# Optimization experiments

Measured on AMD Instinct MI355X. Metric: run time of the kernel, lower is better.

## Reference

```python
import jax, jax.numpy as jnp
import numpy as np

K_CENTERS = 10
G_CENTERS = 2
EPS = 1e-12  # tf.math.l2_normalize epsilon


def setup_inputs() -> dict:
    key = jax.random.key(0)
    k1, k2, k3 = jax.random.split(key, 3)
    B, H, W, D = 16, 16, 64, 512
    KC = K_CENTERS + G_CENTERS
    feat = jax.random.normal(k1, (B, H, W, D), dtype=jnp.float32)
    cluster_score = jax.random.normal(k2, (B, H, W, KC), dtype=jnp.float32)
    cluster = jax.random.normal(k3, (KC, D), dtype=jnp.float32)
    return {"feat": feat, "cluster_score": cluster_score, "cluster": cluster}


def reference(feat, cluster_score, cluster):
    B, H, W, D = feat.shape
    KC = cluster.shape[0]
    # Softmax over clusters (stable)
    A = jax.nn.softmax(cluster_score, axis=-1)            # [B,H,W,KC]
    # Flatten spatial dims: sum_{s} A[b,s,k] * (feat[b,s,d] - cluster[k,d])
    Af = A.reshape(B, H * W, KC)
    ff = feat.reshape(B, H * W, D)
    # = einsum(A, feat) - (sum_s A)[b,k] * cluster[k,d]  (avoids [B,S,KC,D] intermediate)
    cluster_res = jnp.einsum('bsk,bsd->bkd', Af, ff) - Af.sum(axis=1)[..., None] * cluster[None]
    # GhostVLAD: keep only real clusters
    cluster_res = cluster_res[:, :K_CENTERS, :]           # [B,K,D]
    # L2 normalize over feature dim
    sq = jnp.sum(cluster_res * cluster_res, axis=-1, keepdims=True)
    cluster_l2 = cluster_res * jax.lax.rsqrt(jnp.maximum(sq, EPS))
    return cluster_l2.reshape(B, K_CENTERS * D)
```

## Files before the change

### kernel.cpp

```cpp
#include <hip/hip_runtime.h>
#include <hip/hip_bf16.h>


#define B_   16
#define S_   1024
#define D_   512
#define KC_  12
#define K_   10
#define CH_  16
#define SCH_ (S_ / CH_)
#define NT1  512
#define NPAR 4

__global__ __launch_bounds__(NT1) void vlad_accum(
    const float* __restrict__ feat, const float* __restrict__ score,
    float* __restrict__ part, float* __restrict__ asum_part)
{
    const int bid = blockIdx.x;
    const int b = bid / CH_, c = bid % CH_;
    const int s0 = c * SCH_;
    const int tid = threadIdx.x;
    const int par = tid >> 7;
    const int col = tid & 127;

    __shared__ float A[SCH_][KC_];
    __shared__ float red[NPAR - 1][K_ * 4][128];

    if (tid < SCH_) {
        const float4* sp = (const float4*)(score + (size_t)(b * S_ + s0 + tid) * KC_);
        const float4 w0 = sp[0], w1 = sp[1], w2 = sp[2];
        float x[KC_] = {w0.x, w0.y, w0.z, w0.w, w1.x, w1.y, w1.z, w1.w,
                        w2.x, w2.y, w2.z, w2.w};
        float m = x[0];
        #pragma unroll
        for (int k = 1; k < KC_; k++) m = fmaxf(m, x[k]);
        float sum = 0.f;
        #pragma unroll
        for (int k = 0; k < KC_; k++) { x[k] = __expf(x[k] - m); sum += x[k]; }
        const float inv = 1.0f / sum;
        #pragma unroll
        for (int k = 0; k < KC_; k++) A[tid][k] = x[k] * inv;
    }
    __syncthreads();

    if (tid < K_) {
        float v = 0.f;
        #pragma unroll
        for (int s = 0; s < SCH_; s++) v += A[s][tid];
        asum_part[(b * CH_ + c) * K_ + tid] = v;
    }

    float acc[K_][4];
    #pragma unroll
    for (int k = 0; k < K_; k++)
        acc[k][0] = acc[k][1] = acc[k][2] = acc[k][3] = 0.f;

    const float4* fp = (const float4*)(feat + (size_t)(b * S_ + s0) * D_) + col;
    #pragma unroll 8
    for (int i = 0; i < SCH_ / NPAR; i++) {
        const int s = NPAR * i + par;
        const float4 v = fp[(size_t)s * (D_ / 4)];
        const float4 a0 = *(const float4*)(&A[s][0]);
        const float4 a1 = *(const float4*)(&A[s][4]);
        const float2 a2 = *(const float2*)(&A[s][8]);
        const float a[K_] = {a0.x, a0.y, a0.z, a0.w, a1.x, a1.y, a1.z, a1.w,
                             a2.x, a2.y};
        #pragma unroll
        for (int k = 0; k < K_; k++) {
            acc[k][0] += a[k] * v.x;
            acc[k][1] += a[k] * v.y;
            acc[k][2] += a[k] * v.z;
            acc[k][3] += a[k] * v.w;
        }
    }

    if (par) {
        float (* const r)[128] = red[par - 1];
        #pragma unroll
        for (int k = 0; k < K_; k++) {
            r[k * 4 + 0][col] = acc[k][0];
            r[k * 4 + 1][col] = acc[k][1];
            r[k * 4 + 2][col] = acc[k][2];
            r[k * 4 + 3][col] = acc[k][3];
        }
    }
    __syncthreads();
    if (!par) {
        float* pp = part + (((size_t)(b * K_) * CH_ + c) * D_) + col * 4;
        #pragma unroll
        for (int k = 0; k < K_; k++) {
            float v0 = acc[k][0], v1 = acc[k][1], v2 = acc[k][2], v3 = acc[k][3];
            #pragma unroll
            for (int p = 0; p < NPAR - 1; p++) {
                v0 += red[p][k * 4 + 0][col];
                v1 += red[p][k * 4 + 1][col];
                v2 += red[p][k * 4 + 2][col];
                v3 += red[p][k * 4 + 3][col];
            }
            *(float4*)(pp + (size_t)k * CH_ * D_) = make_float4(v0, v1, v2, v3);
        }
    }
}

__global__ __launch_bounds__(256) void vlad_final(
    const float* __restrict__ part, const float* __restrict__ asum_part,
    const float* __restrict__ cluster, float* __restrict__ out)
{
    const int b = blockIdx.x / K_;
    const int k = blockIdx.x % K_;
    const int tid = threadIdx.x;
    const int d = tid * 2;

    const float* base = part + ((size_t)(b * K_ + k) * CH_) * D_ + d;
    float s0 = 0.f, s1 = 0.f;
    #pragma unroll 8
    for (int c = 0; c < CH_; c++) {
        const float2 v = *(const float2*)(base + (size_t)c * D_);
        s0 += v.x; s1 += v.y;
    }
    float asv = 0.f;
    #pragma unroll
    for (int c = 0; c < CH_; c++) asv += asum_part[(b * CH_ + c) * K_ + k];

    const float2 cv = *(const float2*)(cluster + (size_t)k * D_ + d);
    const float r0 = s0 - asv * cv.x;
    const float r1 = s1 - asv * cv.y;

    float sq = r0 * r0 + r1 * r1;
    #pragma unroll
    for (int off = 32; off > 0; off >>= 1) sq += __shfl_down(sq, off, 64);
    __shared__ float wsum[4];
    if ((tid & 63) == 0) wsum[tid >> 6] = sq;
    __syncthreads();
    const float tot = wsum[0] + wsum[1] + wsum[2] + wsum[3];
    const float scale = rsqrtf(fmaxf(tot, 1e-12f));

    *(float2*)(out + (size_t)(b * K_ + k) * D_ + d) =
        make_float2(r0 * scale, r1 * scale);
}

extern "C" void kernel_launch(void* const* d_in, const int* in_sizes, int n_in,
                              void* d_out, int out_size, void* d_ws, size_t ws_size,
                              hipStream_t stream) {
    const float* feat    = (const float*)d_in[0];
    const float* score   = (const float*)d_in[1];
    const float* cluster = (const float*)d_in[2];
    float* out = (float*)d_out;

    float* part      = (float*)d_ws;
    float* asum_part = part + (size_t)B_ * K_ * CH_ * D_;

    vlad_accum<<<B_ * CH_, NT1, 0, stream>>>(feat, score, part, asum_part);
    vlad_final<<<B_ * K_, 256, 0, stream>>>(part, asum_part, cluster, out);
}
```

Before: 79.20 us.

## Fuse accumulation and normalization into one kernel split by cluster halves

Replaces the two-kernel scheme (a spatially chunked partial accumulation followed by a reduce-and-normalize pass) with one fused kernel. Each block handles a full batch item and half of the real clusters. The block index is mapped so that both halves of a batch share an XCD and can reuse feat through L2. This removes the workspace round trip and the second launch. In exchange the grid drops from 256 to 32 blocks, and each block streams the entire spatial extent serially, which sharply reduces parallelism across CUs.

```diff
diff --git a/kernel.cpp b/kernel.cpp
--- a/kernel.cpp
+++ b/kernel.cpp
@@ -1,5 +1,4 @@
 #include <hip/hip_runtime.h>
-#include <hip/hip_bf16.h>
 
 
 #define B_   16
@@ -7,136 +6,139 @@
 #define D_   512
 #define KC_  12
 #define K_   10
-#define CH_  16
-#define SCH_ (S_ / CH_)
-#define NT1  512
+#define KL_  5
+#define NT   512
 #define NPAR 4
 
-__global__ __launch_bounds__(NT1) void vlad_accum(
+__global__ __launch_bounds__(NT) void vlad_fused(
     const float* __restrict__ feat, const float* __restrict__ score,
-    float* __restrict__ part, float* __restrict__ asum_part)
+    const float* __restrict__ cluster, float* __restrict__ out)
 {
-    const int bid = blockIdx.x;
-    const int b = bid / CH_, c = bid % CH_;
-    const int s0 = c * SCH_;
-    const int tid = threadIdx.x;
-    const int par = tid >> 7;
-    const int col = tid & 127;
+    const int x    = blockIdx.x;
+    const int half = (x >> 3) & 1;
+    const int b    = (x & 7) | ((x >> 4) << 3);
+    const int k0   = half * KL_;
 
-    __shared__ float A[SCH_][KC_];
-    __shared__ float red[NPAR - 1][K_ * 4][128];
+    const int tid  = threadIdx.x;
+    const int lane = tid & 63;
+    const int wave = tid >> 6;
+    const int par  = tid >> 7;
+    const int col  = tid & 127;
 
-    if (tid < SCH_) {
-        const float4* sp = (const float4*)(score + (size_t)(b * S_ + s0 + tid) * KC_);
+    __shared__ float  As[S_][8];
+    __shared__ float4 red[NPAR - 1][KL_][128];
+    __shared__ float  wpart[8][KL_];
+    __shared__ float  asumL[KL_];
+    __shared__ float  wsumL[2][KL_];
+
+    float aw[KL_];
+    #pragma unroll
+    for (int j = 0; j < KL_; j++) aw[j] = 0.f;
+
+    #pragma unroll
+    for (int t = 0; t < 2; t++) {
+        const int s = tid + t * NT;
+        const float4* sp = (const float4*)(score + (size_t)(b * S_ + s) * KC_);
         const float4 w0 = sp[0], w1 = sp[1], w2 = sp[2];
-        float x[KC_] = {w0.x, w0.y, w0.z, w0.w, w1.x, w1.y, w1.z, w1.w,
-                        w2.x, w2.y, w2.z, w2.w};
-        float m = x[0];
+        float xv[KC_] = {w0.x, w0.y, w0.z, w0.w, w1.x, w1.y, w1.z, w1.w,
+                         w2.x, w2.y, w2.z, w2.w};
+        float m = xv[0];
         #pragma unroll
-        for (int k = 1; k < KC_; k++) m = fmaxf(m, x[k]);
+        for (int k = 1; k < KC_; k++) m = fmaxf(m, xv[k]);
         float sum = 0.f;
         #pragma unroll
-        for (int k = 0; k < KC_; k++) { x[k] = __expf(x[k] - m); sum += x[k]; }
+        for (int k = 0; k < KC_; k++) { xv[k] = __expf(xv[k] - m); sum += xv[k]; }
         const float inv = 1.0f / sum;
+        const float a0 = xv[k0] * inv, a1 = xv[k0 + 1] * inv,
+                    a2 = xv[k0 + 2] * inv, a3 = xv[k0 + 3] * inv,
+                    a4 = xv[k0 + 4] * inv;
+        *(float4*)&As[s][0] = make_float4(a0, a1, a2, a3);
+        As[s][4] = a4;
+        aw[0] += a0; aw[1] += a1; aw[2] += a2; aw[3] += a3; aw[4] += a4;
+    }
+    #pragma unroll
+    for (int j = 0; j < KL_; j++) {
+        float r = aw[j];
         #pragma unroll
-        for (int k = 0; k < KC_; k++) A[tid][k] = x[k] * inv;
+        for (int off = 32; off > 0; off >>= 1) r += __shfl_down(r, off, 64);
+        if (lane == 0) wpart[wave][j] = r;
+    }
+    __syncthreads();
+    if (tid < KL_) {
+        float s = 0.f;
+        #pragma unroll
+        for (int w = 0; w < 8; w++) s += wpart[w][tid];
+        asumL[tid] = s;
+    }
+
+    float acc[KL_][4];
+    #pragma unroll
+    for (int k = 0; k < KL_; k++)
+        acc[k][0] = acc[k][1] = acc[k][2] = acc[k][3] = 0.f;
+
+    const float4* fp = (const float4*)(feat + (size_t)b * S_ * D_) + col;
+    #pragma unroll 8
+    for (int i = 0; i < S_ / NPAR; i++) {
+        const int s = (i << 2) | par;
+        const float4 v   = fp[(size_t)s * (D_ / 4)];
+        const float4 a03 = *(const float4*)&As[s][0];
+        const float  a4  = As[s][4];
+        acc[0][0] += a03.x * v.x; acc[0][1] += a03.x * v.y;
+        acc[0][2] += a03.x * v.z; acc[0][3] += a03.x * v.w;
+        acc[1][0] += a03.y * v.x; acc[1][1] += a03.y * v.y;
+        acc[1][2] += a03.y * v.z; acc[1][3] += a03.y * v.w;
+        acc[2][0] += a03.z * v.x; acc[2][1] += a03.z * v.y;
+        acc[2][2] += a03.z * v.z; acc[2][3] += a03.z * v.w;
+        acc[3][0] += a03.w * v.x; acc[3][1] += a03.w * v.y;
+        acc[3][2] += a03.w * v.z; acc[3][3] += a03.w * v.w;
+        acc[4][0] += a4   * v.x; acc[4][1] += a4   * v.y;
+        acc[4][2] += a4   * v.z; acc[4][3] += a4   * v.w;
+    }
+
+    if (par) {
+        #pragma unroll
+        for (int k = 0; k < KL_; k++)
+            red[par - 1][k][col] =
+                make_float4(acc[k][0], acc[k][1], acc[k][2], acc[k][3]);
     }
     __syncthreads();
 
-    if (tid < K_) {
-        float v = 0.f;
+    float r[KL_][4];
+    float sq[KL_];
+    if (!par) {
         #pragma unroll
-        for (int s = 0; s < SCH_; s++) v += A[s][tid];
-        asum_part[(b * CH_ + c) * K_ + tid] = v;
-    }
-
-    float acc[K_][4];
-    #pragma unroll
-    for (int k = 0; k < K_; k++)
-        acc[k][0] = acc[k][1] = acc[k][2] = acc[k][3] = 0.f;
-
-    const float4* fp = (const float4*)(feat + (size_t)(b * S_ + s0) * D_) + col;
-    #pragma unroll 8
-    for (int i = 0; i < SCH_ / NPAR; i++) {
-        const int s = NPAR * i + par;
-        const float4 v = fp[(size_t)s * (D_ / 4)];
-        const float4 a0 = *(const float4*)(&A[s][0]);
-        const float4 a1 = *(const float4*)(&A[s][4]);
-        const float2 a2 = *(const float2*)(&A[s][8]);
-        const float a[K_] = {a0.x, a0.y, a0.z, a0.w, a1.x, a1.y, a1.z, a1.w,
-                             a2.x, a2.y};
+        for (int k = 0; k < KL_; k++) {
+            float v0 = acc[k][0], v1 = acc[k][1], v2 = acc[k][2], v3 = acc[k][3];
+            #pragma unroll
+            for (int p = 0; p < NPAR - 1; p++) {
+                const float4 t = red[p][k][col];
+                v0 += t.x; v1 += t.y; v2 += t.z; v3 += t.w;
+            }
+            const float  asv = asumL[k];
+            const float4 cv  = *(const float4*)(cluster + (size_t)(k0 + k) * D_ + col * 4);
+            v0 -= asv * cv.x; v1 -= asv * cv.y; v2 -= asv * cv.z; v3 -= asv * cv.w;
+            r[k][0] = v0; r[k][1] = v1; r[k][2] = v2; r[k][3] = v3;
+            sq[k] = v0 * v0 + v1 * v1 + v2 * v2 + v3 * v3;
+        }
         #pragma unroll
-        for (int k = 0; k < K_; k++) {
-            acc[k][0] += a[k] * v.x;
-            acc[k][1] += a[k] * v.y;
-            acc[k][2] += a[k] * v.z;
-            acc[k][3] += a[k] * v.w;
-        }
-    }
-
-    if (par) {
-        float (* const r)[128] = red[par - 1];
-        #pragma unroll
-        for (int k = 0; k < K_; k++) {
-            r[k * 4 + 0][col] = acc[k][0];
-            r[k * 4 + 1][col] = acc[k][1];
-            r[k * 4 + 2][col] = acc[k][2];
-            r[k * 4 + 3][col] = acc[k][3];
+        for (int k = 0; k < KL_; k++) {
+            float s = sq[k];
+            #pragma unroll
+            for (int off = 32; off > 0; off >>= 1) s += __shfl_down(s, off, 64);
+            if (lane == 0) wsumL[wave][k] = s;
         }
     }
     __syncthreads();
+
     if (!par) {
-        float* pp = part + (((size_t)(b * K_) * CH_ + c) * D_) + col * 4;
         #pragma unroll
-        for (int k = 0; k < K_; k++) {
-            float v0 = acc[k][0], v1 = acc[k][1], v2 = acc[k][2], v3 = acc[k][3];
-            #pragma unroll
-            for (int p = 0; p < NPAR - 1; p++) {
-                v0 += red[p][k * 4 + 0][col];
-                v1 += red[p][k * 4 + 1][col];
-                v2 += red[p][k * 4 + 2][col];
-                v3 += red[p][k * 4 + 3][col];
-            }
-            *(float4*)(pp + (size_t)k * CH_ * D_) = make_float4(v0, v1, v2, v3);
+        for (int k = 0; k < KL_; k++) {
+            const float tot = wsumL[0][k] + wsumL[1][k];
+            const float sc  = rsqrtf(fmaxf(tot, 1e-12f));
+            *(float4*)(out + (size_t)(b * K_ + k0 + k) * D_ + col * 4) =
+                make_float4(r[k][0] * sc, r[k][1] * sc, r[k][2] * sc, r[k][3] * sc);
         }
     }
-}
-
-__global__ __launch_bounds__(256) void vlad_final(
-    const float* __restrict__ part, const float* __restrict__ asum_part,
-    const float* __restrict__ cluster, float* __restrict__ out)
-{
-    const int b = blockIdx.x / K_;
-    const int k = blockIdx.x % K_;
-    const int tid = threadIdx.x;
-    const int d = tid * 2;
-
-    const float* base = part + ((size_t)(b * K_ + k) * CH_) * D_ + d;
-    float s0 = 0.f, s1 = 0.f;
-    #pragma unroll 8
-    for (int c = 0; c < CH_; c++) {
-        const float2 v = *(const float2*)(base + (size_t)c * D_);
-        s0 += v.x; s1 += v.y;
-    }
-    float asv = 0.f;
-    #pragma unroll
-    for (int c = 0; c < CH_; c++) asv += asum_part[(b * CH_ + c) * K_ + k];
-
-    const float2 cv = *(const float2*)(cluster + (size_t)k * D_ + d);
-    const float r0 = s0 - asv * cv.x;
-    const float r1 = s1 - asv * cv.y;
-
-    float sq = r0 * r0 + r1 * r1;
-    #pragma unroll
-    for (int off = 32; off > 0; off >>= 1) sq += __shfl_down(sq, off, 64);
-    __shared__ float wsum[4];
-    if ((tid & 63) == 0) wsum[tid >> 6] = sq;
-    __syncthreads();
-    const float tot = wsum[0] + wsum[1] + wsum[2] + wsum[3];
-    const float scale = rsqrtf(fmaxf(tot, 1e-12f));
-
-    *(float2*)(out + (size_t)(b * K_ + k) * D_ + d) =
-        make_float2(r0 * scale, r1 * scale);
 }
 
 extern "C" void kernel_launch(void* const* d_in, const int* in_sizes, int n_in,
@@ -146,10 +148,7 @@
     const float* score   = (const float*)d_in[1];
     const float* cluster = (const float*)d_in[2];
     float* out = (float*)d_out;
+    (void)d_ws; (void)ws_size;
 
-    float* part      = (float*)d_ws;
-    float* asum_part = part + (size_t)B_ * K_ * CH_ * D_;
-
-    vlad_accum<<<B_ * CH_, NT1, 0, stream>>>(feat, score, part, asum_part);
-    vlad_final<<<B_ * K_, 256, 0, stream>>>(part, asum_part, cluster, out);
+    vlad_fused<<<B_ * 2, NT, 0, stream>>>(feat, score, cluster, out);
 }
```

Measured after the change: 93.87 us. +18.5%, slower.

## Prefetch all feature rows into registers before softmax and shuffle-reduce cluster sums

Applied to the files above, without the earlier changes.

The accumulation kernel now issues all 16 feature float4 loads per thread up front, before the softmax and barrier, so global-memory latency overlaps the softmax work. The per-cluster assignment sums move from a serial shared-memory loop to wavefront shuffle reductions. The reduction buffer is vectorised to float4, and launch bounds ask for two blocks per CU. The final kernel also issues all partial loads before summing them. The cost is higher register pressure from the 16-entry float4 array plus the accumulators, which may cap occupancy or cause spills.

```diff
diff --git a/kernel.cpp b/kernel.cpp
--- a/kernel.cpp
+++ b/kernel.cpp
@@ -1,5 +1,4 @@
 #include <hip/hip_runtime.h>
-#include <hip/hip_bf16.h>
 
 
 #define B_   16
@@ -11,8 +10,9 @@
 #define SCH_ (S_ / CH_)
 #define NT1  512
 #define NPAR 4
+#define NPX  (SCH_ / NPAR)
 
-__global__ __launch_bounds__(NT1) void vlad_accum(
+__global__ __launch_bounds__(NT1, 2) void vlad_accum(
     const float* __restrict__ feat, const float* __restrict__ score,
     float* __restrict__ part, float* __restrict__ asum_part)
 {
@@ -23,12 +23,22 @@
     const int par = tid >> 7;
     const int col = tid & 127;
 
-    __shared__ float A[SCH_][KC_];
-    __shared__ float red[NPAR - 1][K_ * 4][128];
+    __shared__ float  As[SCH_][KC_];
+    __shared__ float4 red[NPAR - 1][K_][128];
+
+    float4 w0, w1, w2;
+    if (tid < SCH_) {
+        const float4* sp = (const float4*)(score + (size_t)(b * S_ + s0 + tid) * KC_);
+        w0 = sp[0]; w1 = sp[1]; w2 = sp[2];
+    }
+
+    const float4* fp = (const float4*)(feat + (size_t)(b * S_ + s0) * D_) + col;
+    float4 v[NPX];
+    #pragma unroll
+    for (int i = 0; i < NPX; i++)
+        v[i] = fp[(size_t)(NPAR * i + par) * (D_ / 4)];
 
     if (tid < SCH_) {
-        const float4* sp = (const float4*)(score + (size_t)(b * S_ + s0 + tid) * KC_);
-        const float4 w0 = sp[0], w1 = sp[1], w2 = sp[2];
         float x[KC_] = {w0.x, w0.y, w0.z, w0.w, w1.x, w1.y, w1.z, w1.w,
                         w2.x, w2.y, w2.z, w2.w};
         float m = x[0];
@@ -39,50 +49,47 @@
         for (int k = 0; k < KC_; k++) { x[k] = __expf(x[k] - m); sum += x[k]; }
         const float inv = 1.0f / sum;
         #pragma unroll
-        for (int k = 0; k < KC_; k++) A[tid][k] = x[k] * inv;
+        for (int k = 0; k < KC_; k++) {
+            x[k] *= inv;
+            As[tid][k] = x[k];
+        }
+        #pragma unroll
+        for (int k = 0; k < K_; k++) {
+            float r = x[k];
+            #pragma unroll
+            for (int off = 32; off > 0; off >>= 1) r += __shfl_down(r, off, 64);
+            if (tid == 0) asum_part[(b * CH_ + c) * K_ + k] = r;
+        }
     }
     __syncthreads();
-
-    if (tid < K_) {
-        float v = 0.f;
-        #pragma unroll
-        for (int s = 0; s < SCH_; s++) v += A[s][tid];
-        asum_part[(b * CH_ + c) * K_ + tid] = v;
-    }
 
     float acc[K_][4];
     #pragma unroll
     for (int k = 0; k < K_; k++)
         acc[k][0] = acc[k][1] = acc[k][2] = acc[k][3] = 0.f;
 
-    const float4* fp = (const float4*)(feat + (size_t)(b * S_ + s0) * D_) + col;
-    #pragma unroll 8
-    for (int i = 0; i < SCH_ / NPAR; i++) {
+    #pragma unroll
+    for (int i = 0; i < NPX; i++) {
         const int s = NPAR * i + par;
-        const float4 v = fp[(size_t)s * (D_ / 4)];
-        const float4 a0 = *(const float4*)(&A[s][0]);
-        const float4 a1 = *(const float4*)(&A[s][4]);
-        const float2 a2 = *(const float2*)(&A[s][8]);
+        const float4 a0 = *(const float4*)&As[s][0];
+        const float4 a1 = *(const float4*)&As[s][4];
+        const float2 a2 = *(const float2*)&As[s][8];
         const float a[K_] = {a0.x, a0.y, a0.z, a0.w, a1.x, a1.y, a1.z, a1.w,
                              a2.x, a2.y};
         #pragma unroll
         for (int k = 0; k < K_; k++) {
-            acc[k][0] += a[k] * v.x;
-            acc[k][1] += a[k] * v.y;
-            acc[k][2] += a[k] * v.z;
-            acc[k][3] += a[k] * v.w;
+            acc[k][0] += a[k] * v[i].x;
+            acc[k][1] += a[k] * v[i].y;
+            acc[k][2] += a[k] * v[i].z;
+            acc[k][3] += a[k] * v[i].w;
         }
     }
 
     if (par) {
-        float (* const r)[128] = red[par - 1];
         #pragma unroll
-        for (int k = 0; k < K_; k++) {
-            r[k * 4 + 0][col] = acc[k][0];
-            r[k * 4 + 1][col] = acc[k][1];
-            r[k * 4 + 2][col] = acc[k][2];
-            r[k * 4 + 3][col] = acc[k][3];
-        }
+        for (int k = 0; k < K_; k++)
+            red[par - 1][k][col] =
+                make_float4(acc[k][0], acc[k][1], acc[k][2], acc[k][3]);
     }
     __syncthreads();
     if (!par) {
@@ -92,10 +99,8 @@
             float v0 = acc[k][0], v1 = acc[k][1], v2 = acc[k][2], v3 = acc[k][3];
             #pragma unroll
             for (int p = 0; p < NPAR - 1; p++) {
-                v0 += red[p][k * 4 + 0][col];
-                v1 += red[p][k * 4 + 1][col];
-                v2 += red[p][k * 4 + 2][col];
-                v3 += red[p][k * 4 + 3][col];
+                const float4 t = red[p][k][col];
+                v0 += t.x; v1 += t.y; v2 += t.z; v3 += t.w;
             }
             *(float4*)(pp + (size_t)k * CH_ * D_) = make_float4(v0, v1, v2, v3);
         }
@@ -112,15 +117,18 @@
     const int d = tid * 2;
 
     const float* base = part + ((size_t)(b * K_ + k) * CH_) * D_ + d;
-    float s0 = 0.f, s1 = 0.f;
-    #pragma unroll 8
-    for (int c = 0; c < CH_; c++) {
-        const float2 v = *(const float2*)(base + (size_t)c * D_);
-        s0 += v.x; s1 += v.y;
-    }
+    float2 v[CH_];
+    #pragma unroll
+    for (int c = 0; c < CH_; c++)
+        v[c] = *(const float2*)(base + (size_t)c * D_);
+
     float asv = 0.f;
     #pragma unroll
     for (int c = 0; c < CH_; c++) asv += asum_part[(b * CH_ + c) * K_ + k];
+
+    float s0 = 0.f, s1 = 0.f;
+    #pragma unroll
+    for (int c = 0; c < CH_; c++) { s0 += v[c].x; s1 += v[c].y; }
 
     const float2 cv = *(const float2*)(cluster + (size_t)k * D_ + d);
     const float r0 = s0 - asv * cv.x;
```

Result: no change. 80.62 us (+1.8%).
